# Optimization experiments

Measured on AMD Instinct MI355X. Metric: run time of the kernel, lower is better.

The kernel has to match this reference:

```python
import jax, jax.numpy as jnp
from jax import lax
import numpy as np

C_IN, C_OUT, K, STRIDE, PAD = 64, 64, 3, 1, 1
EPS = 1e-5


def setup_inputs() -> dict:
    key = jax.random.key(0)
    ks = jax.random.split(key, 6)
    B, H, W = 4, 128, 128
    x = jax.random.normal(ks[0], (B, C_IN, H, W), jnp.float32)
    # small offset weights -> realistic sub-pixel offsets
    offset_w = jax.random.normal(ks[1], (2 * K * K, C_IN, K, K), jnp.float32) * 0.01
    offset_b = jax.random.normal(ks[2], (2 * K * K,), jnp.float32) * 0.01
    dcn_w = jax.random.normal(ks[3], (C_OUT, C_IN, K, K), jnp.float32) / np.sqrt(C_IN * K * K)
    gamma = jax.random.uniform(ks[4], (C_OUT,), jnp.float32, 0.5, 1.5)
    beta = jax.random.normal(ks[5], (C_OUT,), jnp.float32) * 0.1
    return dict(x=x, offset_w=offset_w, offset_b=offset_b, dcn_w=dcn_w, gamma=gamma, beta=beta)


def _bilinear_sample(xb, py, px):
    # xb: (C,H,W); py,px: (K2,Ho,Wo) absolute sample coords (may be out of bounds)
    H, W = xb.shape[1], xb.shape[2]
    y0 = jnp.floor(py); x0 = jnp.floor(px)
    wy = py - y0  # frac weights
    wx = px - x0

    def gather(yi, xi):
        yc = jnp.clip(yi, 0, H - 1).astype(jnp.int32)
        xc = jnp.clip(xi, 0, W - 1).astype(jnp.int32)
        v = xb[:, yc, xc]  # (C,K2,Ho,Wo)
        valid = ((yi >= 0) & (yi <= H - 1) & (xi >= 0) & (xi <= W - 1)).astype(xb.dtype)
        return v * valid[None]

    return (gather(y0, x0) * ((1 - wy) * (1 - wx))[None]
            + gather(y0, x0 + 1) * ((1 - wy) * wx)[None]
            + gather(y0 + 1, x0) * (wy * (1 - wx))[None]
            + gather(y0 + 1, x0 + 1) * (wy * wx)[None])  # (C,K2,Ho,Wo)


def reference(x, offset_w, offset_b, dcn_w, gamma, beta):
    B, C, H, W = x.shape
    K2 = K * K
    # offset conv (standard conv, NCHW)
    offset = lax.conv_general_dilated(
        x, offset_w, (STRIDE, STRIDE), [(PAD, PAD), (PAD, PAD)],
        dimension_numbers=("NCHW", "OIHW", "NCHW")) + offset_b[None, :, None, None]
    Ho, Wo = offset.shape[2], offset.shape[3]
    off = offset.reshape(B, K2, 2, Ho, Wo)  # interleaved (dy, dx) per tap
    dy, dx = off[:, :, 0], off[:, :, 1]
    # base sampling grid: out_pos*stride - pad + kernel tap index
    hs = (jnp.arange(Ho) * STRIDE - PAD).astype(x.dtype)
    ws = (jnp.arange(Wo) * STRIDE - PAD).astype(x.dtype)
    ki, kj = jnp.meshgrid(jnp.arange(K), jnp.arange(K), indexing="ij")
    ki = ki.reshape(K2).astype(x.dtype)
    kj = kj.reshape(K2).astype(x.dtype)
    py = dy + hs[None, None, :, None] + ki[None, :, None, None]  # (B,K2,Ho,Wo)
    px = dx + ws[None, None, None, :] + kj[None, :, None, None]

    sampled = jax.vmap(_bilinear_sample)(x, py, px)  # (B,C,K2,Ho,Wo)
    out = jnp.einsum("bckhw,ock->bohw", sampled, dcn_w.reshape(dcn_w.shape[0], C, K2))

    # BatchNorm (training-mode batch stats) + ReLU
    mean = out.mean((0, 2, 3))
    var = out.var((0, 2, 3))
    out = (out - mean[None, :, None, None]) * lax.rsqrt(var + EPS)[None, :, None, None]
    out = out * gamma[None, :, None, None] + beta[None, :, None, None]
    return jnp.maximum(out, 0.0)
```

## Files before the change

kernel.cpp:

```cpp
#include <hip/hip_runtime.h>

#define HW   16384
#define NPX  65536

typedef unsigned short u16;
typedef unsigned int   u32;
typedef short bf16x8 __attribute__((ext_vector_type(8)));
typedef float f32x4  __attribute__((ext_vector_type(4)));

__device__ __forceinline__ u16 f2b(float f) {
    u32 u = __float_as_uint(f);
    return (u16)((u + 0x7FFFu + ((u >> 16) & 1u)) >> 16);
}
__device__ __forceinline__ float blo(u32 u) { return __uint_as_float(u << 16); }
__device__ __forceinline__ float bhi(u32 u) { return __uint_as_float(u & 0xffff0000u); }

__device__ __forceinline__ u32 comb(u32 a00, u32 a01, u32 a10, u32 a11,
                                    float w00, float w01, float w10, float w11) {
    float lo = fmaf(w11, blo(a11), fmaf(w10, blo(a10), fmaf(w01, blo(a01), w00 * blo(a00))));
    float hi = fmaf(w11, bhi(a11), fmaf(w10, bhi(a10), fmaf(w01, bhi(a01), w00 * bhi(a00))));
    return ((__float_as_uint(lo) + 0x8000u) >> 16) | ((__float_as_uint(hi) + 0x8000u) & 0xffff0000u);
}

#define MFMA __builtin_amdgcn_mfma_f32_16x16x32_bf16

__global__ __launch_bounds__(256)
void k_pre(const float* __restrict__ x, const float* __restrict__ dw,
           const float* __restrict__ ow, u16* __restrict__ xh,
           u16* __restrict__ wtd, u16* __restrict__ wto) {
    int tid = threadIdx.x;
    if (blockIdx.x >= 1024) {
        int gid = (blockIdx.x - 1024) * 256 + tid;
        if (gid >= 108 * 64) return;
        int fid = gid >> 6, lane = gid & 63;
        int mi = lane & 15, quad = lane >> 4;
        u32 w[4];
        if (fid < 72) {
            int tap = fid >> 3, rem = fid & 7;
            int ks = rem >> 2, nt = rem & 3;
            int n = nt * 16 + mi;
            int cb = ks * 32 + quad * 8;
#pragma unroll
            for (int i = 0; i < 4; ++i) {
                u32 lo = f2b(dw[(n * 64 + cb + 2 * i) * 9 + tap]);
                u32 hi = f2b(dw[(n * 64 + cb + 2 * i + 1) * 9 + tap]);
                w[i] = lo | (hi << 16);
            }
            *((int4*)wtd + (fid << 6) + lane) = make_int4(w[0], w[1], w[2], w[3]);
        } else {
            int f2 = fid - 72;
            int tap = f2 >> 2, rem = f2 & 3;
            int ks = rem >> 1, nt = rem & 1;
            int n = nt * 16 + mi;
            int cb = ks * 32 + quad * 8;
#pragma unroll
            for (int i = 0; i < 4; ++i) {
                u32 lo = (n < 18) ? f2b(ow[(n * 64 + cb + 2 * i) * 9 + tap]) : 0u;
                u32 hi = (n < 18) ? f2b(ow[(n * 64 + cb + 2 * i + 1) * 9 + tap]) : 0u;
                w[i] = lo | (hi << 16);
            }
            *((int4*)wto + (f2 << 6) + lane) = make_int4(w[0], w[1], w[2], w[3]);
        }
        return;
    }
    __shared__ float tile[64][65];
    int p0  = blockIdx.x * 64;
    int b   = p0 >> 14;
    int hw0 = p0 & (HW - 1);
    int c   = tid >> 2;
    int sub = tid & 3;
    const float* src = x + (size_t)(b * 64 + c) * HW + hw0;
#pragma unroll
    for (int i = 0; i < 4; ++i) {
        float4 v = *(const float4*)(src + i * 16 + sub * 4);
        tile[c][i * 16 + sub * 4 + 0] = v.x;
        tile[c][i * 16 + sub * 4 + 1] = v.y;
        tile[c][i * 16 + sub * 4 + 2] = v.z;
        tile[c][i * 16 + sub * 4 + 3] = v.w;
    }
    __syncthreads();

    int px = tid >> 2;
    u32 w1[4], w2[4];
#pragma unroll
    for (int j = 0; j < 4; ++j) {
        int ch = sub * 8 + 2 * j;
        w1[j] = (u32)f2b(tile[ch][px])      | ((u32)f2b(tile[ch + 1][px]) << 16);
        w2[j] = (u32)f2b(tile[ch + 32][px]) | ((u32)f2b(tile[ch + 33][px]) << 16);
    }
    u16* dst = xh + (size_t)(p0 + px) * 64;
    *(int4*)(dst + sub * 8)      = make_int4(w1[0], w1[1], w1[2], w1[3]);
    *(int4*)(dst + 32 + sub * 8) = make_int4(w2[0], w2[1], w2[2], w2[3]);
}

__global__ __launch_bounds__(256, 6)
void k_main(const u16* __restrict__ xh, const u16* __restrict__ wto,
            const u16* __restrict__ wtd, const float* __restrict__ ob,
            float* __restrict__ out, float* __restrict__ sums) {
    __shared__ float offs[2][18][34];
    __shared__ float so[64][33];

    int tid = threadIdx.x;
    int vb  = (blockIdx.x & 7) * 256 + (blockIdx.x >> 3);
    int p0  = vb * 32;
    int b   = p0 >> 14;
    int hw0 = p0 & (HW - 1);
    int y   = hw0 >> 7;
    int x0  = hw0 & 127;
    int wave = tid >> 6, lane = tid & 63;
    int mi = lane & 15, quad = lane >> 4;
    int ks = wave >> 1;
    int m0 = (wave & 1) << 4;
    int xcol = x0 + m0 + mi;
    int koff = ks * 32 + quad * 8;
    const u16* xb = xh + (size_t)b * HW * 64;
    const bf16x8* WO = (const bf16x8*)wto;
    const bf16x8* WD = (const bf16x8*)wtd;

    f32x4 oa0 = {0.f, 0.f, 0.f, 0.f}, oa1 = {0.f, 0.f, 0.f, 0.f};
#pragma unroll
    for (int tap = 0; tap < 9; ++tap) {
        int yy = y + tap / 3 - 1;
        int xx = xcol + tap % 3 - 1;
        int yc = min(max(yy, 0), 127), xc = min(max(xx, 0), 127);
        bool valid = ((unsigned)yy < 128u) && ((unsigned)xx < 128u);
        int4 a = *(const int4*)(xb + ((yc << 7) + xc) * 64 + koff);
        if (!valid) a = make_int4(0, 0, 0, 0);
        bf16x8 af = __builtin_bit_cast(bf16x8, a);
        oa0 = MFMA(af, WO[((tap * 4 + ks * 2 + 0) << 6) + lane], oa0, 0, 0, 0);
        oa1 = MFMA(af, WO[((tap * 4 + ks * 2 + 1) << 6) + lane], oa1, 0, 0, 0);
    }
    {
        float bias0 = (ks == 0) ? ob[mi] : 0.f;
#pragma unroll
        for (int r = 0; r < 4; ++r)
            offs[ks][mi][m0 + quad * 4 + r] = oa0[r] + bias0;
        if (mi < 2) {
            float bias1 = (ks == 0) ? ob[16 + mi] : 0.f;
#pragma unroll
            for (int r = 0; r < 4; ++r)
                offs[ks][16 + mi][m0 + quad * 4 + r] = oa1[r] + bias1;
        }
    }
    __syncthreads();

    f32x4 acc0 = {0.f,0.f,0.f,0.f}, acc1 = {0.f,0.f,0.f,0.f};
    f32x4 acc2 = {0.f,0.f,0.f,0.f}, acc3 = {0.f,0.f,0.f,0.f};
    int   pxl = m0 + mi;
    float fy = (float)y, fx = (float)xcol;
#pragma unroll
    for (int tap = 0; tap < 9; ++tap) {
        float dy = offs[0][2 * tap][pxl]     + offs[1][2 * tap][pxl];
        float dx = offs[0][2 * tap + 1][pxl] + offs[1][2 * tap + 1][pxl];
        float py  = dy + fy + (float)(tap / 3 - 1);
        float pf  = dx + fx + (float)(tap % 3 - 1);
        float y0f = floorf(py), x0f = floorf(pf);
        float wy  = py - y0f,   wx  = pf - x0f;
        int   iy0 = (int)y0f,   ix0 = (int)x0f;
        float vy0 = (y0f >=  0.f && y0f <= 127.f) ? 1.f : 0.f;
        float vy1 = (y0f >= -1.f && y0f <= 126.f) ? 1.f : 0.f;
        float vx0 = (x0f >=  0.f && x0f <= 127.f) ? 1.f : 0.f;
        float vx1 = (x0f >= -1.f && x0f <= 126.f) ? 1.f : 0.f;
        int cy0 = min(max(iy0, 0), 127), cy1 = min(max(iy0 + 1, 0), 127);
        int cx0 = min(max(ix0, 0), 127), cx1 = min(max(ix0 + 1, 0), 127);
        float w00 = (1.f - wy) * (1.f - wx) * vy0 * vx0;
        float w01 = (1.f - wy) * wx * vy0 * vx1;
        float w10 = wy * (1.f - wx) * vy1 * vx0;
        float w11 = wy * wx * vy1 * vx1;
        int4 v00 = *(const int4*)(xb + ((cy0 << 7) + cx0) * 64 + koff);
        int4 v01 = *(const int4*)(xb + ((cy0 << 7) + cx1) * 64 + koff);
        int4 v10 = *(const int4*)(xb + ((cy1 << 7) + cx0) * 64 + koff);
        int4 v11 = *(const int4*)(xb + ((cy1 << 7) + cx1) * 64 + koff);
        int4 r;
        r.x = comb(v00.x, v01.x, v10.x, v11.x, w00, w01, w10, w11);
        r.y = comb(v00.y, v01.y, v10.y, v11.y, w00, w01, w10, w11);
        r.z = comb(v00.z, v01.z, v10.z, v11.z, w00, w01, w10, w11);
        r.w = comb(v00.w, v01.w, v10.w, v11.w, w00, w01, w10, w11);
        bf16x8 a = __builtin_bit_cast(bf16x8, r);
        acc0 = MFMA(a, WD[((tap * 8 + ks * 4 + 0) << 6) + lane], acc0, 0, 0, 0);
        acc1 = MFMA(a, WD[((tap * 8 + ks * 4 + 1) << 6) + lane], acc1, 0, 0, 0);
        acc2 = MFMA(a, WD[((tap * 8 + ks * 4 + 2) << 6) + lane], acc2, 0, 0, 0);
        acc3 = MFMA(a, WD[((tap * 8 + ks * 4 + 3) << 6) + lane], acc3, 0, 0, 0);
    }

    if (ks == 1) {
#pragma unroll
        for (int r = 0; r < 4; ++r) {
            so[ 0 + mi][m0 + quad * 4 + r] = acc0[r];
            so[16 + mi][m0 + quad * 4 + r] = acc1[r];
            so[32 + mi][m0 + quad * 4 + r] = acc2[r];
            so[48 + mi][m0 + quad * 4 + r] = acc3[r];
        }
    }
    __syncthreads();
    if (ks == 0) {
#pragma unroll
        for (int r = 0; r < 4; ++r) {
            so[ 0 + mi][m0 + quad * 4 + r] += acc0[r];
            so[16 + mi][m0 + quad * 4 + r] += acc1[r];
            so[32 + mi][m0 + quad * 4 + r] += acc2[r];
            so[48 + mi][m0 + quad * 4 + r] += acc3[r];
        }
    }
    __syncthreads();

    int n  = tid >> 2;
    int c4 = tid & 3;
    int pl = c4 * 8;
    float s = 0.f, q = 0.f;
    float vals[8];
#pragma unroll
    for (int i = 0; i < 8; ++i) {
        float v = so[n][pl + i];
        vals[i] = v;
        s += v;
        q = fmaf(v, v, q);
    }
    float* dst = out + (size_t)(b * 64 + n) * HW + (y << 7) + x0 + pl;
    *(float4*)dst       = make_float4(vals[0], vals[1], vals[2], vals[3]);
    *(float4*)(dst + 4) = make_float4(vals[4], vals[5], vals[6], vals[7]);

    s += __shfl_xor(s, 1); s += __shfl_xor(s, 2);
    q += __shfl_xor(q, 1); q += __shfl_xor(q, 2);
    if (c4 == 0) {
        float* sb = sums + (blockIdx.x & 7) * 128;
        atomicAdd(&sb[n], s);
        atomicAdd(&sb[64 + n], q);
    }
}

__global__ __launch_bounds__(256)
void k_bn(float* __restrict__ out, const float* __restrict__ sums,
          const float* __restrict__ gamma, const float* __restrict__ beta) {
    int i4 = blockIdx.x * 256 + threadIdx.x;
    int e  = i4 << 2;
    int o  = (e >> 14) & 63;
    float sm = 0.f, sq = 0.f;
#pragma unroll
    for (int s8 = 0; s8 < 8; ++s8) {
        sm += sums[s8 * 128 + o];
        sq += sums[s8 * 128 + 64 + o];
    }
    const float n = 65536.f;
    float mean = sm / n;
    float var  = fmaxf(sq / n - mean * mean, 0.f);
    float sc   = rsqrtf(var + 1e-5f) * gamma[o];
    float sh   = beta[o] - mean * sc;
    float4 v = *(const float4*)&out[e];
    v.x = fmaxf(fmaf(v.x, sc, sh), 0.f);
    v.y = fmaxf(fmaf(v.y, sc, sh), 0.f);
    v.z = fmaxf(fmaf(v.z, sc, sh), 0.f);
    v.w = fmaxf(fmaf(v.w, sc, sh), 0.f);
    *(float4*)&out[e] = v;
}

extern "C" void kernel_launch(void* const* d_in, const int* in_sizes, int n_in,
                              void* d_out, int out_size, void* d_ws, size_t ws_size,
                              hipStream_t stream) {
    const float* x     = (const float*)d_in[0];
    const float* ow    = (const float*)d_in[1];
    const float* ob    = (const float*)d_in[2];
    const float* dw    = (const float*)d_in[3];
    const float* gamma = (const float*)d_in[4];
    const float* beta  = (const float*)d_in[5];
    float* out = (float*)d_out;
    char*  wsb = (char*)d_ws;
    u16*   xh   = (u16*)wsb;
    u16*   wtd  = (u16*)(wsb + 8388608);
    u16*   wto  = (u16*)(wsb + 8462336);
    float* sums = (float*)(wsb + 8499200);

    hipMemsetAsync(sums, 0, 8 * 128 * sizeof(float), stream);
    k_pre<<<1051, 256, 0, stream>>>(x, dw, ow, xh, wtd, wto);
    k_main<<<2048, 256, 0, stream>>>(xh, wto, wtd, ob, out, sums);
    k_bn<<<4096, 256, 0, stream>>>(out, sums, gamma, beta);
}
```

Baseline: 143.0 us.

## Software-pipeline deformable sampling loads, fold memset into prepass, rework transpose

The bilinear-sampling loop now prefetches the next tap's four gathered vectors and weight fragments before combining and issuing MFMAs on the current tap, with a sched_barrier to keep the order. The offset-conv loads are all hoisted ahead of their MFMAs. The prepass converts to bf16 before staging in shared memory and handles 128 pixels per block. The separate memset of the BN sums is folded into a spare block of the prepass, and launch bounds drop occupancy from 6 to 4 waves to make room for the extra registers. The aim is to hide gather latency and cut launch overhead, at the cost of more register pressure and fewer resident waves.

```diff
diff --git a/kernel.cpp b/kernel.cpp
--- a/kernel.cpp
+++ b/kernel.cpp
@@ -21,16 +21,31 @@
     float hi = fmaf(w11, bhi(a11), fmaf(w10, bhi(a10), fmaf(w01, bhi(a01), w00 * bhi(a00))));
     return ((__float_as_uint(lo) + 0x8000u) >> 16) | ((__float_as_uint(hi) + 0x8000u) & 0xffff0000u);
 }
+__device__ __forceinline__ bf16x8 comb4(int4 v00, int4 v01, int4 v10, int4 v11,
+                                        float w00, float w01, float w10, float w11) {
+    int4 r;
+    r.x = comb(v00.x, v01.x, v10.x, v11.x, w00, w01, w10, w11);
+    r.y = comb(v00.y, v01.y, v10.y, v11.y, w00, w01, w10, w11);
+    r.z = comb(v00.z, v01.z, v10.z, v11.z, w00, w01, w10, w11);
+    r.w = comb(v00.w, v01.w, v10.w, v11.w, w00, w01, w10, w11);
+    return __builtin_bit_cast(bf16x8, r);
+}
 
 #define MFMA __builtin_amdgcn_mfma_f32_16x16x32_bf16
 
 __global__ __launch_bounds__(256)
 void k_pre(const float* __restrict__ x, const float* __restrict__ dw,
            const float* __restrict__ ow, u16* __restrict__ xh,
-           u16* __restrict__ wtd, u16* __restrict__ wto) {
+           u16* __restrict__ wtd, u16* __restrict__ wto,
+           float* __restrict__ sums) {
     int tid = threadIdx.x;
-    if (blockIdx.x >= 1024) {
-        int gid = (blockIdx.x - 1024) * 256 + tid;
+    int bid = blockIdx.x;
+    if (bid >= 512) {
+        if (bid == 539) {
+            for (int i = tid; i < 1024; i += 256) sums[i] = 0.f;
+            return;
+        }
+        int gid = (bid - 512) * 256 + tid;
         if (gid >= 108 * 64) return;
         int fid = gid >> 6, lane = gid & 63;
         int mi = lane & 15, quad = lane >> 4;
@@ -63,37 +78,39 @@
         }
         return;
     }
-    __shared__ float tile[64][65];
-    int p0  = blockIdx.x * 64;
+    __shared__ u16 tile[64][138];
+    int p0  = bid * 128;
     int b   = p0 >> 14;
     int hw0 = p0 & (HW - 1);
-    int c   = tid >> 2;
+    int pxq = (tid & 31) * 4;
+    int rr  = tid >> 5;
+    const float* src = x + (size_t)b * 64 * HW + hw0 + pxq;
+#pragma unroll
+    for (int i = 0; i < 8; ++i) {
+        int c = i * 8 + rr;
+        float4 v = *(const float4*)(src + (size_t)c * HW);
+        ushort4 h;
+        h.x = f2b(v.x); h.y = f2b(v.y); h.z = f2b(v.z); h.w = f2b(v.w);
+        *(ushort4*)&tile[c][pxq] = h;
+    }
+    __syncthreads();
     int sub = tid & 3;
-    const float* src = x + (size_t)(b * 64 + c) * HW + hw0;
-#pragma unroll
-    for (int i = 0; i < 4; ++i) {
-        float4 v = *(const float4*)(src + i * 16 + sub * 4);
-        tile[c][i * 16 + sub * 4 + 0] = v.x;
-        tile[c][i * 16 + sub * 4 + 1] = v.y;
-        tile[c][i * 16 + sub * 4 + 2] = v.z;
-        tile[c][i * 16 + sub * 4 + 3] = v.w;
-    }
-    __syncthreads();
-
-    int px = tid >> 2;
-    u32 w1[4], w2[4];
-#pragma unroll
-    for (int j = 0; j < 4; ++j) {
-        int ch = sub * 8 + 2 * j;
-        w1[j] = (u32)f2b(tile[ch][px])      | ((u32)f2b(tile[ch + 1][px]) << 16);
-        w2[j] = (u32)f2b(tile[ch + 32][px]) | ((u32)f2b(tile[ch + 33][px]) << 16);
-    }
-    u16* dst = xh + (size_t)(p0 + px) * 64;
-    *(int4*)(dst + sub * 8)      = make_int4(w1[0], w1[1], w1[2], w1[3]);
-    *(int4*)(dst + 32 + sub * 8) = make_int4(w2[0], w2[1], w2[2], w2[3]);
-}
-
-__global__ __launch_bounds__(256, 6)
+#pragma unroll
+    for (int j = 0; j < 2; ++j) {
+        int px = j * 64 + (tid >> 2);
+        u32 w[8];
+#pragma unroll
+        for (int t = 0; t < 8; ++t) {
+            int c = sub * 16 + 2 * t;
+            w[t] = (u32)tile[c][px] | ((u32)tile[c + 1][px] << 16);
+        }
+        u16* dst = xh + (size_t)(p0 + px) * 64 + sub * 16;
+        *(int4*)dst       = make_int4(w[0], w[1], w[2], w[3]);
+        *(int4*)(dst + 8) = make_int4(w[4], w[5], w[6], w[7]);
+    }
+}
+
+__global__ __launch_bounds__(256, 4)
 void k_main(const u16* __restrict__ xh, const u16* __restrict__ wto,
             const u16* __restrict__ wtd, const float* __restrict__ ob,
             float* __restrict__ out, float* __restrict__ sums) {
@@ -117,16 +134,21 @@
     const bf16x8* WO = (const bf16x8*)wto;
     const bf16x8* WD = (const bf16x8*)wtd;
 
-    f32x4 oa0 = {0.f, 0.f, 0.f, 0.f}, oa1 = {0.f, 0.f, 0.f, 0.f};
+    int4 av[9];
 #pragma unroll
     for (int tap = 0; tap < 9; ++tap) {
         int yy = y + tap / 3 - 1;
         int xx = xcol + tap % 3 - 1;
         int yc = min(max(yy, 0), 127), xc = min(max(xx, 0), 127);
-        bool valid = ((unsigned)yy < 128u) && ((unsigned)xx < 128u);
         int4 a = *(const int4*)(xb + ((yc << 7) + xc) * 64 + koff);
-        if (!valid) a = make_int4(0, 0, 0, 0);
-        bf16x8 af = __builtin_bit_cast(bf16x8, a);
+        if (!(((unsigned)yy < 128u) && ((unsigned)xx < 128u)))
+            a = make_int4(0, 0, 0, 0);
+        av[tap] = a;
+    }
+    f32x4 oa0 = {0.f, 0.f, 0.f, 0.f}, oa1 = {0.f, 0.f, 0.f, 0.f};
+#pragma unroll
+    for (int tap = 0; tap < 9; ++tap) {
+        bf16x8 af = __builtin_bit_cast(bf16x8, av[tap]);
         oa0 = MFMA(af, WO[((tap * 4 + ks * 2 + 0) << 6) + lane], oa0, 0, 0, 0);
         oa1 = MFMA(af, WO[((tap * 4 + ks * 2 + 1) << 6) + lane], oa1, 0, 0, 0);
     }
@@ -144,16 +166,17 @@
     }
     __syncthreads();
 
-    f32x4 acc0 = {0.f,0.f,0.f,0.f}, acc1 = {0.f,0.f,0.f,0.f};
-    f32x4 acc2 = {0.f,0.f,0.f,0.f}, acc3 = {0.f,0.f,0.f,0.f};
-    int   pxl = m0 + mi;
+    int pxl = m0 + mi;
+    float offv[18];
+#pragma unroll
+    for (int m = 0; m < 18; ++m)
+        offv[m] = offs[0][m][pxl] + offs[1][m][pxl];
+
     float fy = (float)y, fx = (float)xcol;
-#pragma unroll
-    for (int tap = 0; tap < 9; ++tap) {
-        float dy = offs[0][2 * tap][pxl]     + offs[1][2 * tap][pxl];
-        float dx = offs[0][2 * tap + 1][pxl] + offs[1][2 * tap + 1][pxl];
-        float py  = dy + fy + (float)(tap / 3 - 1);
-        float pf  = dx + fx + (float)(tap % 3 - 1);
+    auto coords = [&](int tap, float& w00, float& w01, float& w10, float& w11,
+                      int& o00, int& o01, int& o10, int& o11) {
+        float py  = offv[2 * tap]     + fy + (float)(tap / 3 - 1);
+        float pf  = offv[2 * tap + 1] + fx + (float)(tap % 3 - 1);
         float y0f = floorf(py), x0f = floorf(pf);
         float wy  = py - y0f,   wx  = pf - x0f;
         int   iy0 = (int)y0f,   ix0 = (int)x0f;
@@ -163,24 +186,57 @@
         float vx1 = (x0f >= -1.f && x0f <= 126.f) ? 1.f : 0.f;
         int cy0 = min(max(iy0, 0), 127), cy1 = min(max(iy0 + 1, 0), 127);
         int cx0 = min(max(ix0, 0), 127), cx1 = min(max(ix0 + 1, 0), 127);
-        float w00 = (1.f - wy) * (1.f - wx) * vy0 * vx0;
-        float w01 = (1.f - wy) * wx * vy0 * vx1;
-        float w10 = wy * (1.f - wx) * vy1 * vx0;
-        float w11 = wy * wx * vy1 * vx1;
-        int4 v00 = *(const int4*)(xb + ((cy0 << 7) + cx0) * 64 + koff);
-        int4 v01 = *(const int4*)(xb + ((cy0 << 7) + cx1) * 64 + koff);
-        int4 v10 = *(const int4*)(xb + ((cy1 << 7) + cx0) * 64 + koff);
-        int4 v11 = *(const int4*)(xb + ((cy1 << 7) + cx1) * 64 + koff);
-        int4 r;
-        r.x = comb(v00.x, v01.x, v10.x, v11.x, w00, w01, w10, w11);
-        r.y = comb(v00.y, v01.y, v10.y, v11.y, w00, w01, w10, w11);
-        r.z = comb(v00.z, v01.z, v10.z, v11.z, w00, w01, w10, w11);
-        r.w = comb(v00.w, v01.w, v10.w, v11.w, w00, w01, w10, w11);
-        bf16x8 a = __builtin_bit_cast(bf16x8, r);
-        acc0 = MFMA(a, WD[((tap * 8 + ks * 4 + 0) << 6) + lane], acc0, 0, 0, 0);
-        acc1 = MFMA(a, WD[((tap * 8 + ks * 4 + 1) << 6) + lane], acc1, 0, 0, 0);
-        acc2 = MFMA(a, WD[((tap * 8 + ks * 4 + 2) << 6) + lane], acc2, 0, 0, 0);
-        acc3 = MFMA(a, WD[((tap * 8 + ks * 4 + 3) << 6) + lane], acc3, 0, 0, 0);
+        w00 = (1.f - wy) * (1.f - wx) * vy0 * vx0;
+        w01 = (1.f - wy) * wx * vy0 * vx1;
+        w10 = wy * (1.f - wx) * vy1 * vx0;
+        w11 = wy * wx * vy1 * vx1;
+        o00 = ((cy0 << 7) + cx0) * 64 + koff;
+        o01 = ((cy0 << 7) + cx1) * 64 + koff;
+        o10 = ((cy1 << 7) + cx0) * 64 + koff;
+        o11 = ((cy1 << 7) + cx1) * 64 + koff;
+    };
+
+    f32x4 acc0 = {0.f,0.f,0.f,0.f}, acc1 = {0.f,0.f,0.f,0.f};
+    f32x4 acc2 = {0.f,0.f,0.f,0.f}, acc3 = {0.f,0.f,0.f,0.f};
+
+    float w00, w01, w10, w11;
+    int   o00, o01, o10, o11;
+    coords(0, w00, w01, w10, w11, o00, o01, o10, o11);
+    int4 v00 = *(const int4*)(xb + o00);
+    int4 v01 = *(const int4*)(xb + o01);
+    int4 v10 = *(const int4*)(xb + o10);
+    int4 v11 = *(const int4*)(xb + o11);
+    bf16x8 b0 = WD[((ks * 4 + 0) << 6) + lane];
+    bf16x8 b1 = WD[((ks * 4 + 1) << 6) + lane];
+    bf16x8 b2 = WD[((ks * 4 + 2) << 6) + lane];
+    bf16x8 b3 = WD[((ks * 4 + 3) << 6) + lane];
+
+#pragma unroll
+    for (int tap = 0; tap < 9; ++tap) {
+        float nw00 = w00, nw01 = w01, nw10 = w10, nw11 = w11;
+        int4 nv00 = v00, nv01 = v01, nv10 = v10, nv11 = v11;
+        bf16x8 nb0 = b0, nb1 = b1, nb2 = b2, nb3 = b3;
+        if (tap < 8) {
+            int no00, no01, no10, no11;
+            coords(tap + 1, nw00, nw01, nw10, nw11, no00, no01, no10, no11);
+            nv00 = *(const int4*)(xb + no00);
+            nv01 = *(const int4*)(xb + no01);
+            nv10 = *(const int4*)(xb + no10);
+            nv11 = *(const int4*)(xb + no11);
+            nb0 = WD[(((tap + 1) * 8 + ks * 4 + 0) << 6) + lane];
+            nb1 = WD[(((tap + 1) * 8 + ks * 4 + 1) << 6) + lane];
+            nb2 = WD[(((tap + 1) * 8 + ks * 4 + 2) << 6) + lane];
+            nb3 = WD[(((tap + 1) * 8 + ks * 4 + 3) << 6) + lane];
+        }
+        __builtin_amdgcn_sched_barrier(0);
+        bf16x8 a = comb4(v00, v01, v10, v11, w00, w01, w10, w11);
+        acc0 = MFMA(a, b0, acc0, 0, 0, 0);
+        acc1 = MFMA(a, b1, acc1, 0, 0, 0);
+        acc2 = MFMA(a, b2, acc2, 0, 0, 0);
+        acc3 = MFMA(a, b3, acc3, 0, 0, 0);
+        w00 = nw00; w01 = nw01; w10 = nw10; w11 = nw11;
+        v00 = nv00; v01 = nv01; v10 = nv10; v11 = nv11;
+        b0 = nb0; b1 = nb1; b2 = nb2; b3 = nb3;
     }
 
     if (ks == 1) {
@@ -270,8 +326,7 @@
     u16*   wto  = (u16*)(wsb + 8462336);
     float* sums = (float*)(wsb + 8499200);
 
-    hipMemsetAsync(sums, 0, 8 * 128 * sizeof(float), stream);
-    k_pre<<<1051, 256, 0, stream>>>(x, dw, ow, xh, wtd, wto);
+    k_pre<<<540, 256, 0, stream>>>(x, dw, ow, xh, wtd, wto, sums);
     k_main<<<2048, 256, 0, stream>>>(xh, wto, wtd, ob, out, sums);
     k_bn<<<4096, 256, 0, stream>>>(out, sums, gamma, beta);
 }
```

New measurement: 142.3 us. About the same (-0.5%).
